# Kernel optimization log

Hardware: AMD Instinct MI355X
Metric: run time of the kernel (lower is better)

Reference implementation:

```python
import jax, jax.numpy as jnp
import numpy as np

NUM_HEADS = 16
HIDDEN = 64  # per-head dim


def setup_inputs() -> dict:
    key = jax.random.key(0)
    ks = jax.random.split(key, 7)
    B, Nq, S, D = 2, 2048, 2048, 1024
    return {
        "queries": jax.random.normal(ks[0], (B, Nq, D), jnp.float32),
        "keys": jax.random.normal(ks[1], (B, S, D), jnp.float32),
        "values": jax.random.normal(ks[2], (B, S, D), jnp.float32),
        "Wq": jax.random.normal(ks[3], (D, NUM_HEADS * HIDDEN), jnp.float32) * 0.02,
        "Wk": jax.random.normal(ks[4], (D, NUM_HEADS * HIDDEN), jnp.float32) * 0.02,
        "Wv": jax.random.normal(ks[5], (D, NUM_HEADS * HIDDEN), jnp.float32) * 0.02,
        "Wo": jax.random.normal(ks[6], (NUM_HEADS * HIDDEN, 1024), jnp.float32) * 0.02,
    }


def reference(queries, keys, values, Wq, Wk, Wv, Wo):
    B, Nq, _ = queries.shape
    S = keys.shape[1]
    H, dh = NUM_HEADS, HIDDEN
    # projections, split heads: [B, len, H, dh] -> [B, H, len, dh]
    Q = (queries @ Wq).reshape(B, Nq, H, dh).transpose(0, 2, 1, 3)
    K = (keys @ Wk).reshape(B, S, H, dh).transpose(0, 2, 1, 3)
    V = (values @ Wv).reshape(B, S, H, dh).transpose(0, 2, 1, 3)
    scores = jnp.einsum("bhqd,bhkd->bhqk", Q, K) / jnp.sqrt(jnp.float32(dh))
    # NOTE: faithful to original -- softmax over ALL keys, THEN multiply by
    # strictly-lower-triangular mask (triangular * (1 - diagonal)); no renorm.
    P = jax.nn.softmax(scores, axis=-1)
    mask = jnp.tril(jnp.ones((Nq, S), jnp.float32), -1)  # strict lower triangle
    Sout = jnp.einsum("bhqk,bhkd->bhqd", P * mask, V)
    merged = Sout.transpose(0, 2, 1, 3).reshape(B, Nq, H * dh)
    return merged @ Wo
```

## Files before the change

kernel.cpp:

```cpp
#include <hip/hip_runtime.h>
#include <hip/hip_bf16.h>
#include <stdint.h>


typedef __bf16 bf16x8 __attribute__((ext_vector_type(8)));
typedef float f32x4 __attribute__((ext_vector_type(4)));

typedef const __attribute__((address_space(1))) void* gas_t;
typedef __attribute__((address_space(3))) void* las_t;

__device__ __forceinline__ unsigned short f2bf(float f) {
    unsigned int u = __float_as_uint(f);
    return (unsigned short)((u + 0x7FFFu + ((u >> 16) & 1u)) >> 16);
}

__global__ __launch_bounds__(256) void cast_qkv(
    const float* __restrict__ q, const float* __restrict__ k, const float* __restrict__ v,
    unsigned short* __restrict__ oq, unsigned short* __restrict__ ok, unsigned short* __restrict__ ov)
{
    const float* src = (blockIdx.z == 0) ? q : (blockIdx.z == 1) ? k : v;
    unsigned short* dst = (blockIdx.z == 0) ? oq : (blockIdx.z == 1) ? ok : ov;
    unsigned int i = blockIdx.x * 256u + threadIdx.x;
    float4 f = reinterpret_cast<const float4*>(src)[i];
    ushort4 o;
    o.x = f2bf(f.x); o.y = f2bf(f.y); o.z = f2bf(f.z); o.w = f2bf(f.w);
    reinterpret_cast<ushort4*>(dst)[i] = o;
}

__global__ __launch_bounds__(256) void transpose_w(
    const float* __restrict__ w0, const float* __restrict__ w1,
    const float* __restrict__ w2, const float* __restrict__ w3,
    unsigned short* __restrict__ t0, unsigned short* __restrict__ t1,
    unsigned short* __restrict__ t2, unsigned short* __restrict__ t3)
{
    const float* W = (blockIdx.z == 0) ? w0 : (blockIdx.z == 1) ? w1 : (blockIdx.z == 2) ? w2 : w3;
    unsigned short* T = (blockIdx.z == 0) ? t0 : (blockIdx.z == 1) ? t1 : (blockIdx.z == 2) ? t2 : t3;
    __shared__ float s[32][33];
    const int tx = threadIdx.x, ty = threadIdx.y;
    const int x = blockIdx.x * 32 + tx;
#pragma unroll
    for (int j = 0; j < 4; ++j)
        s[ty + 8 * j][tx] = W[(size_t)(blockIdx.y * 32 + ty + 8 * j) * 1024 + x];
    __syncthreads();
    const int xo = blockIdx.y * 32 + tx;
#pragma unroll
    for (int j = 0; j < 4; ++j)
        T[(size_t)(blockIdx.x * 32 + ty + 8 * j) * 1024 + xo] = f2bf(s[tx][ty + 8 * j]);
}

__global__ __launch_bounds__(256) void transpose_v(
    const unsigned short* __restrict__ Vp, unsigned short* __restrict__ Vt)
{
    __shared__ unsigned short s[64][68];
    const int tid = threadIdx.x;
    const int s0 = blockIdx.x * 64, h = blockIdx.y, b = blockIdx.z;
    const size_t inbase = ((size_t)(b * 2048 + s0)) * 1024 + h * 64;
#pragma unroll
    for (int r = 0; r < 4; ++r) {
        int idx = r * 256 + tid;
        int row = idx >> 4;
        int c4 = (idx & 15) * 4;
        ushort4 v = *(const ushort4*)(Vp + inbase + (size_t)row * 1024 + c4);
        *(ushort4*)&s[row][c4] = v;
    }
    __syncthreads();
    const size_t outbase = ((size_t)((b * 16 + h) * 64)) * 2048 + s0;
#pragma unroll
    for (int r = 0; r < 4; ++r) {
        int idx = r * 256 + tid;
        int drow = idx >> 4;
        int sc = (idx & 15) * 4;
        ushort4 v;
        v.x = s[sc][drow]; v.y = s[sc + 1][drow]; v.z = s[sc + 2][drow]; v.w = s[sc + 3][drow];
        *(ushort4*)(Vt + outbase + (size_t)drow * 2048 + sc) = v;
    }
}

template <int BM, int BN, int MODE>
__global__ __launch_bounds__(256) void gemm_bt(
    const unsigned short* __restrict__ A0, const unsigned short* __restrict__ A1,
    const unsigned short* __restrict__ A2,
    const unsigned short* __restrict__ B0, const unsigned short* __restrict__ B1,
    const unsigned short* __restrict__ B2,
    unsigned short* __restrict__ C0, unsigned short* __restrict__ C1,
    unsigned short* __restrict__ C2, float* __restrict__ Cf)
{
    constexpr int K = 1024;
    constexpr int WM = BM / 2, WN = BN / 2, MI = WM / 16, NI = WN / 16;
    __shared__ __align__(16) unsigned char lds[(BM + BN) * 64];
    unsigned char* lA = lds;
    unsigned char* lB = lds + BM * 64;

    const int tid = threadIdx.x;
    const int z = blockIdx.z;
    const unsigned short* A  = (MODE == 1 || z == 0) ? A0 : (z == 1) ? A1 : A2;
    const unsigned short* Bt = (MODE == 1 || z == 0) ? B0 : (z == 1) ? B1 : B2;
    const int m0 = blockIdx.y * BM, n0 = blockIdx.x * BN;
    const int w = tid >> 6, lane = tid & 63, g = lane >> 4, l15 = lane & 15;
    const int wr = w >> 1, wc = w & 1;

    f32x4 acc[MI][NI] = {};

    for (int k0 = 0; k0 < K; k0 += 32) {
#pragma unroll
        for (int r = 0; r < (BM * 64) / 4096; ++r) {
            const int o = (r * 256 + tid) * 16;
            const unsigned char* gp = (const unsigned char*)A
                + ((size_t)(m0 + (o >> 6)) * K + k0) * 2 + (o & 63);
            __builtin_amdgcn_global_load_lds((gas_t)gp,
                (las_t)(lA + (r * 256 + (tid & ~63)) * 16), 16, 0, 0);
        }
#pragma unroll
        for (int r = 0; r < (BN * 64) / 4096; ++r) {
            const int o = (r * 256 + tid) * 16;
            const unsigned char* gp = (const unsigned char*)Bt
                + ((size_t)(n0 + (o >> 6)) * K + k0) * 2 + (o & 63);
            __builtin_amdgcn_global_load_lds((gas_t)gp,
                (las_t)(lB + (r * 256 + (tid & ~63)) * 16), 16, 0, 0);
        }
        __syncthreads();

        bf16x8 a[MI], bfr[NI];
#pragma unroll
        for (int mi = 0; mi < MI; ++mi)
            a[mi] = *(const bf16x8*)(lA + (wr * WM + mi * 16 + l15) * 64 + g * 16);
#pragma unroll
        for (int ni = 0; ni < NI; ++ni)
            bfr[ni] = *(const bf16x8*)(lB + (wc * WN + ni * 16 + l15) * 64 + g * 16);
#pragma unroll
        for (int mi = 0; mi < MI; ++mi)
#pragma unroll
            for (int ni = 0; ni < NI; ++ni)
                acc[mi][ni] = __builtin_amdgcn_mfma_f32_16x16x32_bf16(a[mi], bfr[ni], acc[mi][ni], 0, 0, 0);
        __syncthreads();
    }

    if (MODE == 1) {
#pragma unroll
        for (int mi = 0; mi < MI; ++mi)
#pragma unroll
            for (int ni = 0; ni < NI; ++ni)
#pragma unroll
                for (int i = 0; i < 4; ++i) {
                    const int row = m0 + wr * WM + mi * 16 + 4 * g + i;
                    const int col = n0 + wc * WN + ni * 16 + l15;
                    Cf[(size_t)row * 1024 + col] = acc[mi][ni][i];
                }
    } else {
        unsigned short* C = (z == 0) ? C0 : (z == 1) ? C1 : C2;
#pragma unroll
        for (int mi = 0; mi < MI; ++mi)
#pragma unroll
            for (int ni = 0; ni < NI; ++ni)
#pragma unroll
                for (int i = 0; i < 4; ++i) {
                    const int row = m0 + wr * WM + mi * 16 + 4 * g + i;
                    const int col = n0 + wc * WN + ni * 16 + l15;
                    C[(size_t)row * 1024 + col] = f2bf(acc[mi][ni][i]);
                }
    }
}

__device__ __forceinline__ f32x4 qk_exp(const unsigned char* base, int rowoff,
                                        int ni, int g, int l15,
                                        bf16x8 aq0, bf16x8 aq1)
{
    const int row = rowoff + ni * 16 + l15;
    const int sw = (row & 7) << 4;
    const bf16x8 bk0 = *(const bf16x8*)(base + ((row * 128 + g * 16) ^ sw));
    const bf16x8 bk1 = *(const bf16x8*)(base + ((row * 128 + 64 + g * 16) ^ sw));
    f32x4 t = {};
    t = __builtin_amdgcn_mfma_f32_16x16x32_bf16(bk0, aq0, t, 0, 0, 0);
    t = __builtin_amdgcn_mfma_f32_16x16x32_bf16(bk1, aq1, t, 0, 0, 0);
    f32x4 r;
#pragma unroll
    for (int i = 0; i < 4; ++i) r[i] = __expf(t[i] * 0.125f);
    return r;
}

__global__ __launch_bounds__(256) void attn_kernel(
    const unsigned short* __restrict__ Qp, const unsigned short* __restrict__ Kp,
    const unsigned short* __restrict__ Vt, unsigned short* __restrict__ mrg)
{
    __shared__ __align__(16) unsigned char lds[24576];
    __shared__ float dden[4][16];
    unsigned char* Ks = lds;
    unsigned char* Vs = lds + 8192;
    unsigned char* Ps = lds + 16384;

    const int tid = threadIdx.x;
    const int w = tid >> 6, lane = tid & 63, g = lane >> 4, l15 = lane & 15;
    const int bid = blockIdx.x;
    const int bh = (bid & 7) * 4 + ((bid >> 3) & 3);
    const int qt = 31 - (bid >> 5);
    const int b = bh >> 4, h = bh & 15;
    const int q0 = qt * 64;

    bf16x8 aq0, aq1;
    {
        const unsigned short* qp = Qp + ((size_t)(b * 2048 + q0 + 16 * w + l15) * 1024 + h * 64 + g * 8);
        aq0 = *(const bf16x8*)qp;
        aq1 = *(const bf16x8*)(qp + 32);
    }

    const unsigned char* Kbase = (const unsigned char*)Kp + ((size_t)(b * 2048) * 1024 + h * 64) * 2;
    const unsigned char* Vbase = (const unsigned char*)Vt + ((size_t)bh * 64) * 2048 * 2;

    const int o0 = tid * 16,         r0 = o0 >> 7;
    const int o1 = (256 + tid) * 16, r1 = o1 >> 7;
    const int o2 = (512 + tid) * 16, r2 = o2 >> 7;
    const int o3 = (768 + tid) * 16, r3 = o3 >> 7;

    f32x4 oacc[4] = {};
    f32x4 dsum = {0.f, 0.f, 0.f, 0.f};

    uint4 kr0, kr1, vr0, vr1, cr0, cr1, cr2, cr3;
    kr0 = *(const uint4*)(Kbase + (size_t)r0 * 2048 + (o0 & 127));
    kr1 = *(const uint4*)(Kbase + (size_t)r1 * 2048 + (o1 & 127));
    vr0 = *(const uint4*)(Vbase + (size_t)r0 * 4096 + (o0 & 127));
    vr1 = *(const uint4*)(Vbase + (size_t)r1 * 4096 + (o1 & 127));

    for (int t = 0; t <= qt; ++t) {
        __syncthreads();
        *(uint4*)(Ks + (o0 ^ ((r0 & 7) << 4))) = kr0;
        *(uint4*)(Ks + (o1 ^ ((r1 & 7) << 4))) = kr1;
        *(uint4*)(Vs + (o0 ^ ((r0 & 7) << 4))) = vr0;
        *(uint4*)(Vs + (o1 ^ ((r1 & 7) << 4))) = vr1;
        if (t < qt) {
            const int k1 = (t + 1) * 64;
            kr0 = *(const uint4*)(Kbase + (size_t)(k1 + r0) * 2048 + (o0 & 127));
            kr1 = *(const uint4*)(Kbase + (size_t)(k1 + r1) * 2048 + (o1 & 127));
            vr0 = *(const uint4*)(Vbase + (size_t)r0 * 4096 + (size_t)k1 * 2 + (o0 & 127));
            vr1 = *(const uint4*)(Vbase + (size_t)r1 * 4096 + (size_t)k1 * 2 + (o1 & 127));
        } else if (qt < 31) {
            const int kc = (qt + 1) * 64;
            const int nk = 2048 - kc;
            cr0 = *(const uint4*)(Kbase + (size_t)(kc + r0) * 2048 + (o0 & 127));
            cr1 = *(const uint4*)(Kbase + (size_t)(kc + r1) * 2048 + (o1 & 127));
            if (nk > 64) {
                cr2 = *(const uint4*)(Kbase + (size_t)(kc + r2) * 2048 + (o2 & 127));
                cr3 = *(const uint4*)(Kbase + (size_t)(kc + r3) * 2048 + (o3 & 127));
            }
        }
        __syncthreads();

        f32x4 pe[4];
#pragma unroll
        for (int ni = 0; ni < 4; ++ni) {
            pe[ni] = qk_exp(Ks, 0, ni, g, l15, aq0, aq1);
            dsum += pe[ni];
        }
        if (t == qt) {
            const int qloc = 16 * w + l15;
#pragma unroll
            for (int ni = 0; ni < 4; ++ni)
#pragma unroll
                for (int i = 0; i < 4; ++i)
                    if (ni * 16 + 4 * g + i >= qloc) pe[ni][i] = 0.f;
        }
        {
            const int prow = 16 * w + l15;
            const int pbase = prow * 128;
            const int sw = (prow & 7) << 4;
#pragma unroll
            for (int ni = 0; ni < 4; ++ni) {
                unsigned int lo, hi;
                asm("v_cvt_pk_bf16_f32 %0, %1, %2" : "=v"(lo) : "v"(pe[ni][0]), "v"(pe[ni][1]));
                asm("v_cvt_pk_bf16_f32 %0, %1, %2" : "=v"(hi) : "v"(pe[ni][2]), "v"(pe[ni][3]));
                uint2 pv; pv.x = lo; pv.y = hi;
                *(uint2*)(Ps + ((pbase + ni * 32 + g * 8) ^ sw)) = pv;
            }
        }
#pragma unroll
        for (int kk = 0; kk < 2; ++kk) {
            const int rowp = 16 * w + l15;
            const bf16x8 pa = *(const bf16x8*)(Ps + ((rowp * 128 + kk * 64 + g * 16) ^ ((rowp & 7) << 4)));
#pragma unroll
            for (int ni = 0; ni < 4; ++ni) {
                const int rv = ni * 16 + l15;
                const bf16x8 bv = *(const bf16x8*)(Vs + ((rv * 128 + kk * 64 + g * 16) ^ ((rv & 7) << 4)));
                oacc[ni] = __builtin_amdgcn_mfma_f32_16x16x32_bf16(pa, bv, oacc[ni], 0, 0, 0);
            }
        }
    }

    for (int kc = (qt + 1) * 64; kc < 2048; kc += 128) {
        const int nk = min(128, 2048 - kc);
        __syncthreads();
        *(uint4*)(lds + (o0 ^ ((r0 & 7) << 4))) = cr0;
        *(uint4*)(lds + (o1 ^ ((r1 & 7) << 4))) = cr1;
        if (nk > 64) {
            *(uint4*)(lds + (o2 ^ ((r2 & 7) << 4))) = cr2;
            *(uint4*)(lds + (o3 ^ ((r3 & 7) << 4))) = cr3;
        }
        const int kn = kc + 128;
        if (kn < 2048) {
            const int nk2 = 2048 - kn;
            cr0 = *(const uint4*)(Kbase + (size_t)(kn + r0) * 2048 + (o0 & 127));
            cr1 = *(const uint4*)(Kbase + (size_t)(kn + r1) * 2048 + (o1 & 127));
            if (nk2 > 64) {
                cr2 = *(const uint4*)(Kbase + (size_t)(kn + r2) * 2048 + (o2 & 127));
                cr3 = *(const uint4*)(Kbase + (size_t)(kn + r3) * 2048 + (o3 & 127));
            }
        }
        __syncthreads();
        for (int koff = 0; koff < nk; koff += 64)
#pragma unroll
            for (int ni = 0; ni < 4; ++ni)
                dsum += qk_exp(lds, koff, ni, g, l15, aq0, aq1);
    }

    float den = dsum[0] + dsum[1] + dsum[2] + dsum[3];
    den += __shfl_xor(den, 16, 64);
    den += __shfl_xor(den, 32, 64);
    if (lane < 16) dden[w][lane] = den;
    float inv[4];
#pragma unroll
    for (int i = 0; i < 4; ++i) inv[i] = 1.0f / dden[w][4 * g + i];
#pragma unroll
    for (int ni = 0; ni < 4; ++ni)
#pragma unroll
        for (int i = 0; i < 4; ++i) {
            const int row = q0 + 16 * w + 4 * g + i;
            mrg[((size_t)b * 2048 + row) * 1024 + h * 64 + ni * 16 + l15] =
                f2bf(oacc[ni][i] * inv[i]);
        }
}

extern "C" void kernel_launch(void* const* d_in, const int* in_sizes, int n_in,
                              void* d_out, int out_size, void* d_ws, size_t ws_size,
                              hipStream_t stream)
{
    const float* q  = (const float*)d_in[0];
    const float* k  = (const float*)d_in[1];
    const float* v  = (const float*)d_in[2];
    const float* Wq = (const float*)d_in[3];
    const float* Wk = (const float*)d_in[4];
    const float* Wv = (const float*)d_in[5];
    const float* Wo = (const float*)d_in[6];
    float* out = (float*)d_out;

    unsigned short* ws = (unsigned short*)d_ws;
    const size_t TEN = (size_t)2 * 2048 * 1024;
    unsigned short* qbf = ws;
    unsigned short* kbf = ws + TEN;
    unsigned short* vbf = ws + 2 * TEN;
    unsigned short* Wqt = ws + 3 * TEN;
    unsigned short* Wkt = Wqt + 1024 * 1024;
    unsigned short* Wvt = Wkt + 1024 * 1024;
    unsigned short* Wot = Wvt + 1024 * 1024;
    unsigned short* Qp  = ws + 4 * TEN;
    unsigned short* Kp  = ws + 5 * TEN;
    unsigned short* Vp  = ws + 6 * TEN;
    unsigned short* Vt  = qbf;
    unsigned short* mrg = kbf;

    cast_qkv<<<dim3(4096, 1, 3), 256, 0, stream>>>(q, k, v, qbf, kbf, vbf);
    transpose_w<<<dim3(32, 32, 4), dim3(32, 8), 0, stream>>>(Wq, Wk, Wv, Wo, Wqt, Wkt, Wvt, Wot);
    gemm_bt<128, 128, 0><<<dim3(8, 32, 3), 256, 0, stream>>>(
        qbf, kbf, vbf, Wqt, Wkt, Wvt, Qp, Kp, Vp, nullptr);
    transpose_v<<<dim3(32, 16, 2), 256, 0, stream>>>(Vp, Vt);
    attn_kernel<<<dim3(1024, 1, 1), 256, 0, stream>>>(Qp, Kp, Vt, mrg);
    gemm_bt<64, 128, 1><<<dim3(8, 64, 1), 256, 0, stream>>>(
        mrg, nullptr, nullptr, Wot, nullptr, nullptr, nullptr, nullptr, nullptr, out);
}
```

Measured before the change: 234.2 us.

## Load K/V fragments directly from global into registers, drop LDS staging

The attention kernel no longer stages K and V tiles through shared memory with block-wide barriers. Each wave now loads its MFMA K and V fragments straight from global memory, relying on L1/L2 for the reuse across the four waves. The 1/sqrt(d) scale is folded into the Q projection epilogue, and the P tile swizzle is changed to a wave-local pattern so no __syncthreads is needed. This removes barrier and LDS traffic, but it also drops the register double-buffered prefetch, so global load latency is less hidden and each wave reads K/V redundantly.

```diff
diff --git a/kernel.cpp b/kernel.cpp
--- a/kernel.cpp
+++ b/kernel.cpp
@@ -5,6 +5,7 @@
 
 typedef __bf16 bf16x8 __attribute__((ext_vector_type(8)));
 typedef float f32x4 __attribute__((ext_vector_type(4)));
+typedef unsigned int u32x4 __attribute__((ext_vector_type(4)));
 
 typedef const __attribute__((address_space(1))) void* gas_t;
 typedef __attribute__((address_space(3))) void* las_t;
@@ -148,6 +149,7 @@
                 }
     } else {
         unsigned short* C = (z == 0) ? C0 : (z == 1) ? C1 : C2;
+        const float qscale = (z == 0) ? 0.125f : 1.0f;
 #pragma unroll
         for (int mi = 0; mi < MI; ++mi)
 #pragma unroll
@@ -156,158 +158,113 @@
                 for (int i = 0; i < 4; ++i) {
                     const int row = m0 + wr * WM + mi * 16 + 4 * g + i;
                     const int col = n0 + wc * WN + ni * 16 + l15;
-                    C[(size_t)row * 1024 + col] = f2bf(acc[mi][ni][i]);
+                    C[(size_t)row * 1024 + col] = f2bf(acc[mi][ni][i] * qscale);
                 }
     }
-}
-
-__device__ __forceinline__ f32x4 qk_exp(const unsigned char* base, int rowoff,
-                                        int ni, int g, int l15,
-                                        bf16x8 aq0, bf16x8 aq1)
-{
-    const int row = rowoff + ni * 16 + l15;
-    const int sw = (row & 7) << 4;
-    const bf16x8 bk0 = *(const bf16x8*)(base + ((row * 128 + g * 16) ^ sw));
-    const bf16x8 bk1 = *(const bf16x8*)(base + ((row * 128 + 64 + g * 16) ^ sw));
-    f32x4 t = {};
-    t = __builtin_amdgcn_mfma_f32_16x16x32_bf16(bk0, aq0, t, 0, 0, 0);
-    t = __builtin_amdgcn_mfma_f32_16x16x32_bf16(bk1, aq1, t, 0, 0, 0);
-    f32x4 r;
-#pragma unroll
-    for (int i = 0; i < 4; ++i) r[i] = __expf(t[i] * 0.125f);
-    return r;
 }
 
 __global__ __launch_bounds__(256) void attn_kernel(
     const unsigned short* __restrict__ Qp, const unsigned short* __restrict__ Kp,
     const unsigned short* __restrict__ Vt, unsigned short* __restrict__ mrg)
 {
-    __shared__ __align__(16) unsigned char lds[24576];
+    __shared__ __align__(16) unsigned char Ps[8192];
     __shared__ float dden[4][16];
-    unsigned char* Ks = lds;
-    unsigned char* Vs = lds + 8192;
-    unsigned char* Ps = lds + 16384;
 
     const int tid = threadIdx.x;
     const int w = tid >> 6, lane = tid & 63, g = lane >> 4, l15 = lane & 15;
     const int bid = blockIdx.x;
     const int bh = (bid & 7) * 4 + ((bid >> 3) & 3);
     const int qt = 31 - (bid >> 5);
-    const int b = bh >> 4, h = bh & 15;
+    const int b = bh >> 4, hd = bh & 15;
     const int q0 = qt * 64;
 
     bf16x8 aq0, aq1;
     {
-        const unsigned short* qp = Qp + ((size_t)(b * 2048 + q0 + 16 * w + l15) * 1024 + h * 64 + g * 8);
+        const unsigned short* qp = Qp + ((size_t)(b * 2048 + q0 + 16 * w + l15) * 1024 + hd * 64 + g * 8);
         aq0 = *(const bf16x8*)qp;
         aq1 = *(const bf16x8*)(qp + 32);
     }
 
-    const unsigned char* Kbase = (const unsigned char*)Kp + ((size_t)(b * 2048) * 1024 + h * 64) * 2;
+    const unsigned char* Kbase = (const unsigned char*)Kp + ((size_t)(b * 2048) * 1024 + hd * 64) * 2;
     const unsigned char* Vbase = (const unsigned char*)Vt + ((size_t)bh * 64) * 2048 * 2;
-
-    const int o0 = tid * 16,         r0 = o0 >> 7;
-    const int o1 = (256 + tid) * 16, r1 = o1 >> 7;
-    const int o2 = (512 + tid) * 16, r2 = o2 >> 7;
-    const int o3 = (768 + tid) * 16, r3 = o3 >> 7;
 
     f32x4 oacc[4] = {};
     f32x4 dsum = {0.f, 0.f, 0.f, 0.f};
 
-    uint4 kr0, kr1, vr0, vr1, cr0, cr1, cr2, cr3;
-    kr0 = *(const uint4*)(Kbase + (size_t)r0 * 2048 + (o0 & 127));
-    kr1 = *(const uint4*)(Kbase + (size_t)r1 * 2048 + (o1 & 127));
-    vr0 = *(const uint4*)(Vbase + (size_t)r0 * 4096 + (o0 & 127));
-    vr1 = *(const uint4*)(Vbase + (size_t)r1 * 4096 + (o1 & 127));
+    const int prow = 16 * w + l15;
+    const int pb   = prow * 128;
+    const int psw  = l15 << 3;
 
     for (int t = 0; t <= qt; ++t) {
-        __syncthreads();
-        *(uint4*)(Ks + (o0 ^ ((r0 & 7) << 4))) = kr0;
-        *(uint4*)(Ks + (o1 ^ ((r1 & 7) << 4))) = kr1;
-        *(uint4*)(Vs + (o0 ^ ((r0 & 7) << 4))) = vr0;
-        *(uint4*)(Vs + (o1 ^ ((r1 & 7) << 4))) = vr1;
-        if (t < qt) {
-            const int k1 = (t + 1) * 64;
-            kr0 = *(const uint4*)(Kbase + (size_t)(k1 + r0) * 2048 + (o0 & 127));
-            kr1 = *(const uint4*)(Kbase + (size_t)(k1 + r1) * 2048 + (o1 & 127));
-            vr0 = *(const uint4*)(Vbase + (size_t)r0 * 4096 + (size_t)k1 * 2 + (o0 & 127));
-            vr1 = *(const uint4*)(Vbase + (size_t)r1 * 4096 + (size_t)k1 * 2 + (o1 & 127));
-        } else if (qt < 31) {
-            const int kc = (qt + 1) * 64;
-            const int nk = 2048 - kc;
-            cr0 = *(const uint4*)(Kbase + (size_t)(kc + r0) * 2048 + (o0 & 127));
-            cr1 = *(const uint4*)(Kbase + (size_t)(kc + r1) * 2048 + (o1 & 127));
-            if (nk > 64) {
-                cr2 = *(const uint4*)(Kbase + (size_t)(kc + r2) * 2048 + (o2 & 127));
-                cr3 = *(const uint4*)(Kbase + (size_t)(kc + r3) * 2048 + (o3 & 127));
-            }
-        }
-        __syncthreads();
+        const int k0 = t * 64;
+        bf16x8 kf[4][2], vf[4][2];
+#pragma unroll
+        for (int ni = 0; ni < 4; ++ni) {
+            const unsigned char* kp = Kbase + (size_t)(k0 + ni * 16 + l15) * 2048 + g * 16;
+            kf[ni][0] = *(const bf16x8*)kp;
+            kf[ni][1] = *(const bf16x8*)(kp + 64);
+        }
+#pragma unroll
+        for (int ni = 0; ni < 4; ++ni) {
+            const unsigned char* vp = Vbase + (size_t)(ni * 16 + l15) * 4096 + k0 * 2 + g * 16;
+            vf[ni][0] = *(const bf16x8*)vp;
+            vf[ni][1] = *(const bf16x8*)(vp + 64);
+        }
 
         f32x4 pe[4];
 #pragma unroll
         for (int ni = 0; ni < 4; ++ni) {
-            pe[ni] = qk_exp(Ks, 0, ni, g, l15, aq0, aq1);
+            f32x4 s = {};
+            s = __builtin_amdgcn_mfma_f32_16x16x32_bf16(kf[ni][0], aq0, s, 0, 0, 0);
+            s = __builtin_amdgcn_mfma_f32_16x16x32_bf16(kf[ni][1], aq1, s, 0, 0, 0);
+#pragma unroll
+            for (int i = 0; i < 4; ++i) pe[ni][i] = __expf(s[i]);
             dsum += pe[ni];
         }
         if (t == qt) {
-            const int qloc = 16 * w + l15;
 #pragma unroll
             for (int ni = 0; ni < 4; ++ni)
 #pragma unroll
                 for (int i = 0; i < 4; ++i)
-                    if (ni * 16 + 4 * g + i >= qloc) pe[ni][i] = 0.f;
-        }
-        {
-            const int prow = 16 * w + l15;
-            const int pbase = prow * 128;
-            const int sw = (prow & 7) << 4;
-#pragma unroll
-            for (int ni = 0; ni < 4; ++ni) {
-                unsigned int lo, hi;
-                asm("v_cvt_pk_bf16_f32 %0, %1, %2" : "=v"(lo) : "v"(pe[ni][0]), "v"(pe[ni][1]));
-                asm("v_cvt_pk_bf16_f32 %0, %1, %2" : "=v"(hi) : "v"(pe[ni][2]), "v"(pe[ni][3]));
-                uint2 pv; pv.x = lo; pv.y = hi;
-                *(uint2*)(Ps + ((pbase + ni * 32 + g * 8) ^ sw)) = pv;
-            }
+                    if (ni * 16 + 4 * g + i >= prow) pe[ni][i] = 0.f;
+        }
+#pragma unroll
+        for (int ni = 0; ni < 4; ++ni) {
+            unsigned int lo, hi;
+            asm("v_cvt_pk_bf16_f32 %0, %1, %2" : "=v"(lo) : "v"(pe[ni][0]), "v"(pe[ni][1]));
+            asm("v_cvt_pk_bf16_f32 %0, %1, %2" : "=v"(hi) : "v"(pe[ni][2]), "v"(pe[ni][3]));
+            uint2 pv; pv.x = lo; pv.y = hi;
+            *(uint2*)(Ps + ((pb + ni * 32 + g * 8) ^ psw)) = pv;
         }
 #pragma unroll
         for (int kk = 0; kk < 2; ++kk) {
-            const int rowp = 16 * w + l15;
-            const bf16x8 pa = *(const bf16x8*)(Ps + ((rowp * 128 + kk * 64 + g * 16) ^ ((rowp & 7) << 4)));
-#pragma unroll
-            for (int ni = 0; ni < 4; ++ni) {
-                const int rv = ni * 16 + l15;
-                const bf16x8 bv = *(const bf16x8*)(Vs + ((rv * 128 + kk * 64 + g * 16) ^ ((rv & 7) << 4)));
-                oacc[ni] = __builtin_amdgcn_mfma_f32_16x16x32_bf16(pa, bv, oacc[ni], 0, 0, 0);
-            }
-        }
-    }
-
-    for (int kc = (qt + 1) * 64; kc < 2048; kc += 128) {
-        const int nk = min(128, 2048 - kc);
-        __syncthreads();
-        *(uint4*)(lds + (o0 ^ ((r0 & 7) << 4))) = cr0;
-        *(uint4*)(lds + (o1 ^ ((r1 & 7) << 4))) = cr1;
-        if (nk > 64) {
-            *(uint4*)(lds + (o2 ^ ((r2 & 7) << 4))) = cr2;
-            *(uint4*)(lds + (o3 ^ ((r3 & 7) << 4))) = cr3;
-        }
-        const int kn = kc + 128;
-        if (kn < 2048) {
-            const int nk2 = 2048 - kn;
-            cr0 = *(const uint4*)(Kbase + (size_t)(kn + r0) * 2048 + (o0 & 127));
-            cr1 = *(const uint4*)(Kbase + (size_t)(kn + r1) * 2048 + (o1 & 127));
-            if (nk2 > 64) {
-                cr2 = *(const uint4*)(Kbase + (size_t)(kn + r2) * 2048 + (o2 & 127));
-                cr3 = *(const uint4*)(Kbase + (size_t)(kn + r3) * 2048 + (o3 & 127));
-            }
-        }
-        __syncthreads();
-        for (int koff = 0; koff < nk; koff += 64)
+            const uint2 a0 = *(const uint2*)(Ps + ((pb + kk * 64 + g * 16) ^ psw));
+            const uint2 a1 = *(const uint2*)(Ps + ((pb + kk * 64 + g * 16 + 8) ^ psw));
+            u32x4 au; au.x = a0.x; au.y = a0.y; au.z = a1.x; au.w = a1.y;
+            const bf16x8 pa = *(const bf16x8*)&au;
 #pragma unroll
             for (int ni = 0; ni < 4; ++ni)
-                dsum += qk_exp(lds, koff, ni, g, l15, aq0, aq1);
+                oacc[ni] = __builtin_amdgcn_mfma_f32_16x16x32_bf16(pa, vf[ni][kk], oacc[ni], 0, 0, 0);
+        }
+    }
+
+    for (int t = qt + 1; t < 32; ++t) {
+        const int k0 = t * 64;
+        bf16x8 kf[4][2];
+#pragma unroll
+        for (int ni = 0; ni < 4; ++ni) {
+            const unsigned char* kp = Kbase + (size_t)(k0 + ni * 16 + l15) * 2048 + g * 16;
+            kf[ni][0] = *(const bf16x8*)kp;
+            kf[ni][1] = *(const bf16x8*)(kp + 64);
+        }
+#pragma unroll
+        for (int ni = 0; ni < 4; ++ni) {
+            f32x4 s = {};
+            s = __builtin_amdgcn_mfma_f32_16x16x32_bf16(kf[ni][0], aq0, s, 0, 0, 0);
+            s = __builtin_amdgcn_mfma_f32_16x16x32_bf16(kf[ni][1], aq1, s, 0, 0, 0);
+#pragma unroll
+            for (int i = 0; i < 4; ++i) dsum[i] += __expf(s[i]);
+        }
     }
 
     float den = dsum[0] + dsum[1] + dsum[2] + dsum[3];
@@ -322,7 +279,7 @@
 #pragma unroll
         for (int i = 0; i < 4; ++i) {
             const int row = q0 + 16 * w + 4 * g + i;
-            mrg[((size_t)b * 2048 + row) * 1024 + h * 64 + ni * 16 + l15] =
+            mrg[((size_t)b * 2048 + row) * 1024 + hd * 64 + ni * 16 + l15] =
                 f2bf(oacc[ni][i] * inv[i]);
         }
 }
```

Result: slower. 387.5 us (+65.5%).
